# Optimization experiments

Hardware: AMD Instinct MI355X
Metric: run time of the kernel (lower is better)

## Reference

```python
import jax, jax.numpy as jnp
import numpy as np

B, L, C = 256, 196, 2048   # batch, conv_att_size, conv_feat_size
E, H, A = 512, 512, 512    # input_encoding_size, lstm_size, att_hidden_size
INITRANGE = 0.1


def _uniform(key, shape):
    return jax.random.uniform(key, shape, jnp.float32, -INITRANGE, INITRANGE)


def setup_inputs() -> dict:
    key = jax.random.key(0)
    ks = jax.random.split(key, 16)
    return {
        "xt": jax.random.normal(ks[0], (B, E), jnp.float32),
        "att_seq": jax.random.normal(ks[1], (B, L, C), jnp.float32),
        "h0": jax.random.normal(ks[2], (1, B, H), jnp.float32),
        "c0": jax.random.normal(ks[3], (1, B, H), jnp.float32),
        # LSTM input projections
        "Wi": _uniform(ks[4], (4 * H, E)), "bi": _uniform(ks[5], (4 * H,)),
        "Wh": _uniform(ks[6], (4 * H, H)), "bh": _uniform(ks[7], (4 * H,)),
        "Wz": _uniform(ks[8], (4 * H, C)), "bz": _uniform(ks[9], (4 * H,)),
        # attention MLP
        "Wa": _uniform(ks[10], (A, C)), "ba": _uniform(ks[11], (A,)),
        "Wha": _uniform(ks[12], (A, H)), "bha": _uniform(ks[13], (A,)),
        "Wo": _uniform(ks[14], (1, A)), "bo": _uniform(ks[15], (1,)),
    }


def reference(xt, att_seq, h0, c0, Wi, bi, Wh, bh, Wz, bz, Wa, ba, Wha, bha, Wo, bo):
    pre_h = h0[-1]  # [B, H]
    pre_c = c0[-1]  # [B, H]

    # attention scoring MLP
    att_linear = jnp.einsum('blc,ac->bla', att_seq, Wa) + ba      # [B, L, A]
    h_linear = pre_h @ Wha.T + bha                                 # [B, A]
    att_h = jnp.tanh(att_linear + h_linear[:, None, :])            # [B, L, A]
    scores = jnp.einsum('bla,a->bl', att_h, Wo[0]) + bo[0]         # [B, L]
    conv_weight = jax.nn.softmax(scores, axis=1)                   # [B, L]

    # weighted sum over attention locations -> context z
    z = jnp.einsum('blc,bl->bc', att_seq, conv_weight)             # [B, C]

    # fused LSTM gates
    all_input_sums = (xt @ Wi.T + bi) + (pre_h @ Wh.T + bh) + (z @ Wz.T + bz)  # [B, 4H]
    gates = jax.nn.sigmoid(all_input_sums[:, :3 * H])
    in_gate = gates[:, :H]
    forget_gate = gates[:, H:2 * H]
    out_gate = gates[:, 2 * H:3 * H]
    in_transform = jnp.tanh(all_input_sums[:, 3 * H:])

    next_c = forget_gate * pre_c + in_gate * in_transform
    next_h = out_gate * jnp.tanh(next_c)
    # dropout is identity in eval mode (deterministic baseline)
    return next_h, next_c
```

## Files before the change

kernel.cpp:

```cpp
#include <hip/hip_runtime.h>
#include <stdint.h>

#define B_ 256
#define L_ 196
#define C_ 2048
#define E_ 512
#define H_ 512
#define A_ 512
#define M_ (B_*L_)

typedef __bf16 bf16x8 __attribute__((ext_vector_type(8)));
typedef float  f32x4  __attribute__((ext_vector_type(4)));

__device__ __forceinline__ unsigned short f2bf(float f) {
    union { float f; unsigned int u; } v; v.f = f;
    unsigned int r = 0x7FFFu + ((v.u >> 16) & 1u);
    return (unsigned short)((v.u + r) >> 16);
}

__device__ __forceinline__ unsigned int pk2(float a, float b) {
    return (unsigned int)f2bf(a) | ((unsigned int)f2bf(b) << 16);
}

__device__ __forceinline__ float tanh_fast(float x) {
    float e = __expf(2.f * x);
    return 1.f - 2.f / (e + 1.f);
}

__device__ __forceinline__ void gload_lds16(const void* g, void* s) {
    __builtin_amdgcn_global_load_lds(
        (const __attribute__((address_space(1))) void*)g,
        (__attribute__((address_space(3))) void*)s, 16, 0, 0);
}


__global__ void k_cvt(const float* __restrict__ src, unsigned short* __restrict__ dst, int n4) {
    int i = blockIdx.x * blockDim.x + threadIdx.x;
    if (i < n4) {
        float4 v = ((const float4*)src)[i];
        ushort4 o; o.x = f2bf(v.x); o.y = f2bf(v.y); o.z = f2bf(v.z); o.w = f2bf(v.w);
        ((ushort4*)dst)[i] = o;
    }
}

__global__ void k_build_wcat(const float* __restrict__ Wi, const float* __restrict__ Wh,
                             const float* __restrict__ Wz, const float* __restrict__ bi,
                             const float* __restrict__ bh, const float* __restrict__ bz,
                             unsigned short* __restrict__ wcat, float* __restrict__ bcat) {
    int j = blockIdx.x;
    int t = threadIdx.x;
    for (int g = t; g < 768; g += 256) {
        int k = g * 4;
        const float* src;
        if (k < 512)       src = Wi + j*512 + k;
        else if (k < 1024) src = Wh + j*512 + (k - 512);
        else               src = Wz + j*2048 + (k - 1024);
        float4 v = *(const float4*)src;
        ushort4 o; o.x = f2bf(v.x); o.y = f2bf(v.y); o.z = f2bf(v.z); o.w = f2bf(v.w);
        *(ushort4*)(wcat + (size_t)j*3072 + k) = o;
    }
    if (t == 0) bcat[j] = bi[j] + bh[j] + bz[j];
}

__global__ void k_build_xcat(const float* __restrict__ xt, const float* __restrict__ preh,
                             unsigned short* __restrict__ xcat) {
    int b = blockIdx.x, t = threadIdx.x;
    const float* src = (t < 128) ? (xt + b*512 + t*4) : (preh + b*512 + (t-128)*4);
    int off = (t < 128) ? (t*4) : (512 + (t-128)*4);
    float4 v = *(const float4*)src;
    ushort4 o; o.x = f2bf(v.x); o.y = f2bf(v.y); o.z = f2bf(v.z); o.w = f2bf(v.w);
    *(ushort4*)(xcat + (size_t)b*3072 + off) = o;
}

__global__ void k_hlin(const float* __restrict__ preh, const float* __restrict__ Wha,
                       const float* __restrict__ bha, const float* __restrict__ ba,
                       float* __restrict__ hlin) {
    __shared__ float ph[512];
    int b = blockIdx.x, t = threadIdx.x;
    ph[t] = preh[b*512 + t];
    __syncthreads();
    float acc = bha[t] + ba[t];
    const float4* wrow = (const float4*)(Wha + (size_t)t*512);
    #pragma unroll 8
    for (int k4 = 0; k4 < 128; ++k4) {
        float4 v = wrow[k4];
        float4 p = *(const float4*)&ph[k4*4];
        acc += v.x*p.x + v.y*p.y + v.z*p.z + v.w*p.w;
    }
    hlin[b*512 + t] = acc;
}


#define VWAIT8 asm volatile("s_waitcnt vmcnt(8)" ::: "memory")
#define VWAIT4 asm volatile("s_waitcnt vmcnt(4)" ::: "memory")
#define VWAIT0 asm volatile("s_waitcnt vmcnt(0)" ::: "memory")
#define LWAIT0 asm volatile("s_waitcnt lgkmcnt(0)" ::: "memory")

#define ISSUE_B(K0, LBN) do { \
    _Pragma("unroll") \
    for (int i_ = 0; i_ < 8; ++i_) \
        gload_lds16(wa + (size_t)(brow0 + i_*64)*C_ + (K0) + bpsC*8, \
                    (LBN) + (size_t)(tid + i_*512)*8); \
} while(0)

#define LOAD_A(K0) do { const float* ga_ = gaBase + (K0); \
    av0 = *(const float4*)(ga_);      av1 = *(const float4*)(ga_ + 4); \
    av2 = *(const float4*)(ga_ + 8);  av3 = *(const float4*)(ga_ + 12); \
} while(0)

#define PACK_A(LAN) do { \
    uint4 w0_ = make_uint4(pk2(av0.x,av0.y), pk2(av0.z,av0.w), pk2(av1.x,av1.y), pk2(av1.z,av1.w)); \
    uint4 w1_ = make_uint4(pk2(av2.x,av2.y), pk2(av2.z,av2.w), pk2(av3.x,av3.y), pk2(av3.z,av3.w)); \
    *(uint4*)&(LAN)[ar*64 + ((app     ^ ars) * 8)] = w0_; \
    *(uint4*)&(LAN)[ar*64 + (((app+1) ^ ars) * 8)] = w1_; \
} while(0)

#define COMPUTE(KK, LA, LB) do { \
    const int c_ = (KK)*4 + lq; \
    bf16x8 af_[4]; \
    _Pragma("unroll") \
    for (int m_ = 0; m_ < 4; ++m_) { \
        int rrow_ = wr*64 + m_*16 + l16; \
        af_[m_] = *(const bf16x8*)&(LA)[rrow_*64 + ((c_ ^ (rrow_ & 7)) * 8)]; } \
    __builtin_amdgcn_s_setprio(1); \
    _Pragma("unroll") \
    for (int n_ = 0; n_ < 8; ++n_) { \
        int brow_ = wc*128 + n_*16 + l16; \
        bf16x8 bf_ = *(const bf16x8*)&(LB)[brow_*64 + ((c_ ^ (brow_ & 7)) * 8)]; \
        _Pragma("unroll") \
        for (int m_ = 0; m_ < 4; ++m_) \
            acc[m_][n_] = __builtin_amdgcn_mfma_f32_16x16x32_bf16(af_[m_], bf_, acc[m_][n_], 0, 0, 0); } \
    __builtin_amdgcn_s_setprio(0); \
} while(0)

__global__ __launch_bounds__(512, 1) void k_scores(
    const float* __restrict__ att,
    const unsigned short* __restrict__ wa,
    const float* __restrict__ hlin,
    const float* __restrict__ wo,
    const float* __restrict__ bo,
    float* __restrict__ scores)
{
    __shared__ unsigned short smem[81920];
    const int tid = threadIdx.x;
    const int w = tid >> 6, l = tid & 63;
    const int l16 = l & 15, lq = l >> 4;
    const int wr = w >> 2, wc = w & 3;
    const int row0 = blockIdx.x * 128;

    const int ar = tid >> 2;
    const int app = (tid & 3) * 2;
    const int ars = ar & 7;
    const float* gaBase = att + (size_t)(row0 + ar)*C_ + app*8;

    const int brow0 = tid >> 3;
    const int bpsC = (tid & 7) ^ ((tid >> 3) & 7);

    f32x4 acc[4][8];
    #pragma unroll
    for (int m = 0; m < 4; ++m)
        #pragma unroll
        for (int n = 0; n < 8; ++n) acc[m][n] = (f32x4){0.f, 0.f, 0.f, 0.f};

    float4 av0, av1, av2, av3;
    unsigned short* lA0 = smem;
    unsigned short* lB0 = smem + 8192;
    unsigned short* lA1 = smem + 40960;
    unsigned short* lB1 = smem + 40960 + 8192;

    LOAD_A(0);
    ISSUE_B(0, lB0);
    VWAIT8;
    PACK_A(lA0);
    LOAD_A(64);
    VWAIT4;
    LWAIT0;
    __builtin_amdgcn_s_barrier();

    for (int kt = 0; kt < 30; ++kt) {
        unsigned short* lA  = (kt & 1) ? lA1 : lA0;
        unsigned short* lB  = (kt & 1) ? lB1 : lB0;
        unsigned short* lAn = (kt & 1) ? lA0 : lA1;
        unsigned short* lBn = (kt & 1) ? lB0 : lB1;
        ISSUE_B((kt + 1) * 64, lBn);
        COMPUTE(0, lA, lB);
        VWAIT8;
        PACK_A(lAn);
        COMPUTE(1, lA, lB);
        LOAD_A((kt + 2) * 64);
        VWAIT4;
        LWAIT0;
        __builtin_amdgcn_s_barrier();
    }

    {
        ISSUE_B(31 * 64, lB1);
        COMPUTE(0, lA0, lB0);
        VWAIT8;
        PACK_A(lA1);
        COMPUTE(1, lA0, lB0);
        VWAIT0;
        LWAIT0;
        __builtin_amdgcn_s_barrier();
    }

    COMPUTE(0, lA1, lB1);
    COMPUTE(1, lA1, lB1);

    __syncthreads();
    float* red = (float*)smem;

    const int colbase = wc*128 + l16;
    float won[8], hlA[8], hlB[8];
    const int bA = row0 / L_;
    const int bB = (row0 + 127) / L_;
    const int rsplit = (bA + 1) * L_;
    #pragma unroll
    for (int n = 0; n < 8; ++n) {
        won[n] = wo[colbase + n*16];
        hlA[n] = hlin[bA*A_ + colbase + n*16];
        hlB[n] = hlin[bB*A_ + colbase + n*16];
    }

    #pragma unroll
    for (int m = 0; m < 4; ++m) {
        #pragma unroll
        for (int r = 0; r < 4; ++r) {
            int lrow = wr*64 + m*16 + lq*4 + r;
            int grow = row0 + lrow;
            bool useB = grow >= rsplit;
            float s = 0.f;
            #pragma unroll
            for (int n = 0; n < 8; ++n) {
                float v = acc[m][n][r] + (useB ? hlB[n] : hlA[n]);
                s += tanh_fast(v) * won[n];
            }
            s += __shfl_xor(s, 1);
            s += __shfl_xor(s, 2);
            s += __shfl_xor(s, 4);
            s += __shfl_xor(s, 8);
            if (l16 == 0) red[wc*128 + lrow] = s;
        }
    }
    __syncthreads();
    if (tid < 128) {
        scores[row0 + tid] = red[tid] + red[128 + tid] + red[256 + tid] + red[384 + tid] + bo[0];
    }
}

__global__ void k_softmax(const float* __restrict__ scores, float* __restrict__ cw) {
    __shared__ float sm[4], ss[4];
    int b = blockIdx.x, t = threadIdx.x, w = t >> 6, l = t & 63;
    float v = (t < L_) ? scores[b*L_ + t] : -1e30f;
    float m = v;
    #pragma unroll
    for (int o = 1; o < 64; o <<= 1) m = fmaxf(m, __shfl_xor(m, o));
    if (l == 0) sm[w] = m;
    __syncthreads();
    m = fmaxf(fmaxf(sm[0], sm[1]), fmaxf(sm[2], sm[3]));
    float e = (t < L_) ? expf(v - m) : 0.f;
    float s = e;
    #pragma unroll
    for (int o = 1; o < 64; o <<= 1) s += __shfl_xor(s, o);
    if (l == 0) ss[w] = s;
    __syncthreads();
    s = ss[0] + ss[1] + ss[2] + ss[3];
    if (t < L_) cw[b*L_ + t] = e / s;
}

__global__ void k_z(const float* __restrict__ att, const float* __restrict__ cw,
                    unsigned short* __restrict__ xcat) {
    __shared__ float w_s[L_];
    int b = blockIdx.y, half = blockIdx.x, t = threadIdx.x;
    if (t < L_) w_s[t] = cw[b*L_ + t];
    __syncthreads();
    int c = half*1024 + t*4;
    const float* base = att + (size_t)b*L_*C_ + c;
    float ax = 0.f, ay = 0.f, az = 0.f, aw = 0.f;
    #pragma unroll 4
    for (int li = 0; li < L_; ++li) {
        float4 v = *(const float4*)(base + (size_t)li*C_);
        float wt = w_s[li];
        ax += wt*v.x; ay += wt*v.y; az += wt*v.z; aw += wt*v.w;
    }
    ushort4 o; o.x = f2bf(ax); o.y = f2bf(ay); o.z = f2bf(az); o.w = f2bf(aw);
    *(ushort4*)(xcat + (size_t)b*3072 + 1024 + c) = o;
}

#define K2_LDK 40
__global__ __launch_bounds__(256) void k_gemm2(
    const unsigned short* __restrict__ xcat,
    const unsigned short* __restrict__ wcat,
    const float* __restrict__ bcat,
    float* __restrict__ S)
{
    __shared__ unsigned short lA[64 * K2_LDK];
    __shared__ unsigned short lB[128 * K2_LDK];
    const int tid = threadIdx.x;
    const int w = tid >> 6, l = tid & 63;
    const int l16 = l & 15, lq = l >> 4;
    const int row0 = blockIdx.y * 64;
    const int col0 = blockIdx.x * 128;

    f32x4 acc[4][2];
    #pragma unroll
    for (int m = 0; m < 4; ++m)
        #pragma unroll
        for (int n = 0; n < 2; ++n) acc[m][n] = (f32x4){0.f, 0.f, 0.f, 0.f};

    for (int kt = 0; kt < 3072/32; ++kt) {
        const int k0 = kt * 32;
        __syncthreads();
        {
            int r = tid >> 2, c8 = tid & 3;
            *(uint4*)&lA[r*K2_LDK + c8*8] =
                *(const uint4*)(xcat + (size_t)(row0 + r)*3072 + k0 + c8*8);
        }
        #pragma unroll
        for (int i = 0; i < 2; ++i) {
            int g = tid + i*256;
            int r = g >> 2, c8 = g & 3;
            *(uint4*)&lB[r*K2_LDK + c8*8] =
                *(const uint4*)(wcat + (size_t)(col0 + r)*3072 + k0 + c8*8);
        }
        __syncthreads();

        bf16x8 af[4];
        #pragma unroll
        for (int m = 0; m < 4; ++m)
            af[m] = *(const bf16x8*)&lA[(m*16 + l16)*K2_LDK + lq*8];
        #pragma unroll
        for (int n = 0; n < 2; ++n) {
            bf16x8 bfr = *(const bf16x8*)&lB[(w*32 + n*16 + l16)*K2_LDK + lq*8];
            #pragma unroll
            for (int m = 0; m < 4; ++m)
                acc[m][n] = __builtin_amdgcn_mfma_f32_16x16x32_bf16(af[m], bfr, acc[m][n], 0, 0, 0);
        }
    }

    #pragma unroll
    for (int m = 0; m < 4; ++m)
        #pragma unroll
        for (int n = 0; n < 2; ++n)
            #pragma unroll
            for (int r = 0; r < 4; ++r) {
                int grow = row0 + m*16 + lq*4 + r;
                int col = col0 + w*32 + n*16 + l16;
                S[(size_t)grow*2048 + col] = acc[m][n][r] + bcat[col];
            }
}

__global__ void k_lstm(const float* __restrict__ S, const float* __restrict__ prec,
                       float* __restrict__ out) {
    int b = blockIdx.x, h = threadIdx.x;
    float ig = 1.f / (1.f + expf(-S[(size_t)b*2048 + h]));
    float fg = 1.f / (1.f + expf(-S[(size_t)b*2048 + 512 + h]));
    float og = 1.f / (1.f + expf(-S[(size_t)b*2048 + 1024 + h]));
    float gt = tanhf(S[(size_t)b*2048 + 1536 + h]);
    float c = fg * prec[b*512 + h] + ig * gt;
    out[b*512 + h] = og * tanhf(c);
    out[131072 + b*512 + h] = c;
}

extern "C" void kernel_launch(void* const* d_in, const int* in_sizes, int n_in,
                              void* d_out, int out_size, void* d_ws, size_t ws_size,
                              hipStream_t stream) {
    const float* xt  = (const float*)d_in[0];
    const float* att = (const float*)d_in[1];
    const float* h0  = (const float*)d_in[2];
    const float* c0  = (const float*)d_in[3];
    const float* Wi  = (const float*)d_in[4];
    const float* bi  = (const float*)d_in[5];
    const float* Wh  = (const float*)d_in[6];
    const float* bh  = (const float*)d_in[7];
    const float* Wz  = (const float*)d_in[8];
    const float* bz  = (const float*)d_in[9];
    const float* Wa  = (const float*)d_in[10];
    const float* ba  = (const float*)d_in[11];
    const float* Wha = (const float*)d_in[12];
    const float* bha = (const float*)d_in[13];
    const float* Wo  = (const float*)d_in[14];
    const float* bo  = (const float*)d_in[15];
    float* out = (float*)d_out;

    char* ws = (char*)d_ws;
    unsigned short* wa_bf   = (unsigned short*)(ws);
    unsigned short* wcat_bf = (unsigned short*)(ws + 2097152);
    unsigned short* xcat_bf = (unsigned short*)(ws + 14680064);
    float* hlin   = (float*)(ws + 16252928);
    float* scores = (float*)(ws + 16777216);
    float* cw     = (float*)(ws + 16977920);
    float* bcat   = (float*)(ws + 17178624);
    float* S      = (float*)(ws + 17186816);

    k_cvt<<<1024, 256, 0, stream>>>(Wa, wa_bf, 262144);
    k_build_wcat<<<2048, 256, 0, stream>>>(Wi, Wh, Wz, bi, bh, bz, wcat_bf, bcat);
    k_build_xcat<<<256, 256, 0, stream>>>(xt, h0, xcat_bf);
    k_hlin<<<256, 512, 0, stream>>>(h0, Wha, bha, ba, hlin);
    k_scores<<<M_/128, 512, 0, stream>>>(att, wa_bf, hlin, Wo, bo, scores);
    k_softmax<<<256, 256, 0, stream>>>(scores, cw);
    k_z<<<dim3(2, 256), 256, 0, stream>>>(att, cw, xcat_bf);
    k_gemm2<<<dim3(16, 4), 256, 0, stream>>>(xcat_bf, wcat_bf, bcat, S);
    k_lstm<<<256, 512, 0, stream>>>(S, c0, out);
}
```

Baseline: 343.3 us.

## Split scores GEMM into 128x256 tiles with two column blocks and partial sums

The attention-score GEMM moves from 128x512 tiles with 512 threads and one block per CU to 128x256 tiles with 256 threads, a 32-wide K step, and two blocks per CU. The grid is remapped so that column blocks sharing a row block stay close together. Each column block writes a partial score, and the softmax kernel adds the two partials plus the bias. The aim is higher occupancy and better latency hiding from smaller LDS use. The cost is that the att activations are read and converted to bf16 twice, and each K step is shorter, so there are more barriers.

```diff
diff --git a/kernel.cpp b/kernel.cpp
--- a/kernel.cpp
+++ b/kernel.cpp
@@ -91,70 +91,78 @@
 }
 
 
-#define VWAIT8 asm volatile("s_waitcnt vmcnt(8)" ::: "memory")
 #define VWAIT4 asm volatile("s_waitcnt vmcnt(4)" ::: "memory")
 #define VWAIT0 asm volatile("s_waitcnt vmcnt(0)" ::: "memory")
 #define LWAIT0 asm volatile("s_waitcnt lgkmcnt(0)" ::: "memory")
 
 #define ISSUE_B(K0, LBN) do { \
     _Pragma("unroll") \
-    for (int i_ = 0; i_ < 8; ++i_) \
-        gload_lds16(wa + (size_t)(brow0 + i_*64)*C_ + (K0) + bpsC*8, \
-                    (LBN) + (size_t)(tid + i_*512)*8); \
+    for (int i_ = 0; i_ < 4; ++i_) \
+        gload_lds16(gbBase + (size_t)i_*64*C_ + (K0), \
+                    (LBN) + (size_t)(tid + i_*256)*8); \
 } while(0)
 
-#define LOAD_A(K0) do { const float* ga_ = gaBase + (K0); \
-    av0 = *(const float4*)(ga_);      av1 = *(const float4*)(ga_ + 4); \
-    av2 = *(const float4*)(ga_ + 8);  av3 = *(const float4*)(ga_ + 12); \
+#define LOAD_A(K0) do { \
+    av0 = *(const float4*)(gaBase0 + (K0));      av1 = *(const float4*)(gaBase0 + (K0) + 4); \
+    av2 = *(const float4*)(gaBase1 + (K0));      av3 = *(const float4*)(gaBase1 + (K0) + 4); \
 } while(0)
 
 #define PACK_A(LAN) do { \
     uint4 w0_ = make_uint4(pk2(av0.x,av0.y), pk2(av0.z,av0.w), pk2(av1.x,av1.y), pk2(av1.z,av1.w)); \
     uint4 w1_ = make_uint4(pk2(av2.x,av2.y), pk2(av2.z,av2.w), pk2(av3.x,av3.y), pk2(av3.z,av3.w)); \
-    *(uint4*)&(LAN)[ar*64 + ((app     ^ ars) * 8)] = w0_; \
-    *(uint4*)&(LAN)[ar*64 + (((app+1) ^ ars) * 8)] = w1_; \
+    *(uint4*)&(LAN)[ar0*32 + aqs] = w0_; \
+    *(uint4*)&(LAN)[ar0*32 + 2048 + aqs] = w1_; \
 } while(0)
 
-#define COMPUTE(KK, LA, LB) do { \
-    const int c_ = (KK)*4 + lq; \
+#define COMPUTE(LA, LB) do { \
     bf16x8 af_[4]; \
     _Pragma("unroll") \
-    for (int m_ = 0; m_ < 4; ++m_) { \
-        int rrow_ = wr*64 + m_*16 + l16; \
-        af_[m_] = *(const bf16x8*)&(LA)[rrow_*64 + ((c_ ^ (rrow_ & 7)) * 8)]; } \
+    for (int m_ = 0; m_ < 4; ++m_) \
+        af_[m_] = *(const bf16x8*)&(LA)[(wr*64 + m_*16 + l16)*32 + co]; \
     __builtin_amdgcn_s_setprio(1); \
     _Pragma("unroll") \
     for (int n_ = 0; n_ < 8; ++n_) { \
-        int brow_ = wc*128 + n_*16 + l16; \
-        bf16x8 bf_ = *(const bf16x8*)&(LB)[brow_*64 + ((c_ ^ (brow_ & 7)) * 8)]; \
+        bf16x8 bf_ = *(const bf16x8*)&(LB)[(wc*128 + n_*16 + l16)*32 + co]; \
         _Pragma("unroll") \
         for (int m_ = 0; m_ < 4; ++m_) \
             acc[m_][n_] = __builtin_amdgcn_mfma_f32_16x16x32_bf16(af_[m_], bf_, acc[m_][n_], 0, 0, 0); } \
     __builtin_amdgcn_s_setprio(0); \
 } while(0)
 
-__global__ __launch_bounds__(512, 1) void k_scores(
+__global__ __launch_bounds__(256, 2) void k_scores(
     const float* __restrict__ att,
     const unsigned short* __restrict__ wa,
     const float* __restrict__ hlin,
     const float* __restrict__ wo,
-    const float* __restrict__ bo,
-    float* __restrict__ scores)
+    float* __restrict__ part)
 {
-    __shared__ unsigned short smem[81920];
+    __shared__ unsigned short smem[24576];
     const int tid = threadIdx.x;
     const int w = tid >> 6, l = tid & 63;
     const int l16 = l & 15, lq = l >> 4;
-    const int wr = w >> 2, wc = w & 3;
-    const int row0 = blockIdx.x * 128;
-
-    const int ar = tid >> 2;
-    const int app = (tid & 3) * 2;
-    const int ars = ar & 7;
-    const float* gaBase = att + (size_t)(row0 + ar)*C_ + app*8;
-
-    const int brow0 = tid >> 3;
-    const int bpsC = (tid & 7) ^ ((tid >> 3) & 7);
+    const int wr = w >> 1, wc = w & 1;
+
+    const int orig = blockIdx.x;
+    const int wgid = (orig & 7) * 98 + (orig >> 3);
+    const int rowblk = wgid >> 1, colblk = wgid & 1;
+    const int row0 = rowblk * 128;
+    const int colB0 = colblk * 256;
+
+    const int ar0 = tid >> 2;
+    const int aq = tid & 3;
+    const int asw = (ar0 & 3) ^ ((ar0 >> 2) & 3);
+    const int aqs = ((aq ^ asw) << 3);
+    const float* gaBase0 = att + (size_t)(row0 + ar0)*C_ + aq*8;
+    const float* gaBase1 = gaBase0 + (size_t)64*C_;
+    const unsigned short* gbBase = wa + (size_t)(colB0 + ar0)*C_ + (aq ^ asw)*8;
+
+    const int lsw = (l16 & 3) ^ ((l16 >> 2) & 3);
+    const int co = ((lq ^ lsw) << 3);
+
+    unsigned short* lA0 = smem;
+    unsigned short* lB0 = smem + 4096;
+    unsigned short* lA1 = smem + 12288;
+    unsigned short* lB1 = smem + 12288 + 4096;
 
     f32x4 acc[4][8];
     #pragma unroll
@@ -163,54 +171,45 @@
         for (int n = 0; n < 8; ++n) acc[m][n] = (f32x4){0.f, 0.f, 0.f, 0.f};
 
     float4 av0, av1, av2, av3;
-    unsigned short* lA0 = smem;
-    unsigned short* lB0 = smem + 8192;
-    unsigned short* lA1 = smem + 40960;
-    unsigned short* lB1 = smem + 40960 + 8192;
 
     LOAD_A(0);
     ISSUE_B(0, lB0);
-    VWAIT8;
+    VWAIT4;
     PACK_A(lA0);
-    LOAD_A(64);
+    LOAD_A(32);
     VWAIT4;
     LWAIT0;
     __builtin_amdgcn_s_barrier();
 
-    for (int kt = 0; kt < 30; ++kt) {
+    for (int kt = 0; kt < 62; ++kt) {
         unsigned short* lA  = (kt & 1) ? lA1 : lA0;
         unsigned short* lB  = (kt & 1) ? lB1 : lB0;
         unsigned short* lAn = (kt & 1) ? lA0 : lA1;
         unsigned short* lBn = (kt & 1) ? lB0 : lB1;
-        ISSUE_B((kt + 1) * 64, lBn);
-        COMPUTE(0, lA, lB);
-        VWAIT8;
+        ISSUE_B((kt + 1) * 32, lBn);
+        VWAIT4;
         PACK_A(lAn);
-        COMPUTE(1, lA, lB);
-        LOAD_A((kt + 2) * 64);
+        COMPUTE(lA, lB);
+        LOAD_A((kt + 2) * 32);
         VWAIT4;
         LWAIT0;
         __builtin_amdgcn_s_barrier();
     }
 
-    {
-        ISSUE_B(31 * 64, lB1);
-        COMPUTE(0, lA0, lB0);
-        VWAIT8;
-        PACK_A(lA1);
-        COMPUTE(1, lA0, lB0);
-        VWAIT0;
-        LWAIT0;
-        __builtin_amdgcn_s_barrier();
-    }
-
-    COMPUTE(0, lA1, lB1);
-    COMPUTE(1, lA1, lB1);
+    ISSUE_B(63 * 32, lB1);
+    VWAIT4;
+    PACK_A(lA1);
+    COMPUTE(lA0, lB0);
+    VWAIT0;
+    LWAIT0;
+    __builtin_amdgcn_s_barrier();
+
+    COMPUTE(lA1, lB1);
 
     __syncthreads();
     float* red = (float*)smem;
 
-    const int colbase = wc*128 + l16;
+    const int colbase = colB0 + wc*128 + l16;
     float won[8], hlA[8], hlB[8];
     const int bA = row0 / L_;
     const int bB = (row0 + 127) / L_;
@@ -243,15 +242,19 @@
         }
     }
     __syncthreads();
-    if (tid < 128) {
-        scores[row0 + tid] = red[tid] + red[128 + tid] + red[256 + tid] + red[384 + tid] + bo[0];
-    }
-}
-
-__global__ void k_softmax(const float* __restrict__ scores, float* __restrict__ cw) {
+    if (tid < 128)
+        part[(size_t)colblk*M_ + row0 + tid] = red[tid] + red[128 + tid];
+}
+
+__global__ void k_softmax(const float* __restrict__ part, const float* __restrict__ bo,
+                          float* __restrict__ cw) {
     __shared__ float sm[4], ss[4];
     int b = blockIdx.x, t = threadIdx.x, w = t >> 6, l = t & 63;
-    float v = (t < L_) ? scores[b*L_ + t] : -1e30f;
+    float v = -1e30f;
+    if (t < L_) {
+        int idx = b*L_ + t;
+        v = part[idx] + part[M_ + idx] + bo[0];
+    }
     float m = v;
     #pragma unroll
     for (int o = 1; o < 64; o <<= 1) m = fmaxf(m, __shfl_xor(m, o));
@@ -388,17 +391,17 @@
     unsigned short* wcat_bf = (unsigned short*)(ws + 2097152);
     unsigned short* xcat_bf = (unsigned short*)(ws + 14680064);
     float* hlin   = (float*)(ws + 16252928);
-    float* scores = (float*)(ws + 16777216);
-    float* cw     = (float*)(ws + 16977920);
-    float* bcat   = (float*)(ws + 17178624);
-    float* S      = (float*)(ws + 17186816);
+    float* part   = (float*)(ws + 16777216);
+    float* cw     = (float*)(ws + 17825792);
+    float* bcat   = (float*)(ws + 18087936);
+    float* S      = (float*)(ws + 18096128);
 
     k_cvt<<<1024, 256, 0, stream>>>(Wa, wa_bf, 262144);
     k_build_wcat<<<2048, 256, 0, stream>>>(Wi, Wh, Wz, bi, bh, bz, wcat_bf, bcat);
     k_build_xcat<<<256, 256, 0, stream>>>(xt, h0, xcat_bf);
     k_hlin<<<256, 512, 0, stream>>>(h0, Wha, bha, ba, hlin);
-    k_scores<<<M_/128, 512, 0, stream>>>(att, wa_bf, hlin, Wo, bo, scores);
-    k_softmax<<<256, 256, 0, stream>>>(scores, cw);
+    k_scores<<<784, 256, 0, stream>>>(att, wa_bf, hlin, Wo, part);
+    k_softmax<<<256, 256, 0, stream>>>(part, bo, cw);
     k_z<<<dim3(2, 256), 256, 0, stream>>>(att, cw, xcat_bf);
     k_gemm2<<<dim3(16, 4), 256, 0, stream>>>(xcat_bf, wcat_bf, bcat, S);
     k_lstm<<<256, 512, 0, stream>>>(S, c0, out);
```

Result: slower. 426.5 us (+24.3%).

## Emit bf16 copy of att_seq from scores GEMM and read it in context reduction

Applied to the files above, without the earlier changes.

The scores kernel, which already converts att_seq tiles to bf16 for the MFMA, now also stores those bf16 tiles to a workspace buffer. The context-vector kernel then reads the bf16 copy instead of the fp32 tensor, halving its read traffic. The trade-off is an extra large global write inside the GEMM main loop and reduced precision of the weighted sum inputs.

```diff
diff --git a/kernel.cpp b/kernel.cpp
--- a/kernel.cpp
+++ b/kernel.cpp
@@ -20,6 +20,10 @@
 
 __device__ __forceinline__ unsigned int pk2(float a, float b) {
     return (unsigned int)f2bf(a) | ((unsigned int)f2bf(b) << 16);
+}
+
+__device__ __forceinline__ float bf2f(unsigned int lo16) {
+    union { unsigned int u; float f; } v; v.u = lo16 << 16; return v.f;
 }
 
 __device__ __forceinline__ float tanh_fast(float x) {
@@ -108,11 +112,13 @@
     av2 = *(const float4*)(ga_ + 8);  av3 = *(const float4*)(ga_ + 12); \
 } while(0)
 
-#define PACK_A(LAN) do { \
+#define PACK_STORE_A(LAN, KN) do { \
     uint4 w0_ = make_uint4(pk2(av0.x,av0.y), pk2(av0.z,av0.w), pk2(av1.x,av1.y), pk2(av1.z,av1.w)); \
     uint4 w1_ = make_uint4(pk2(av2.x,av2.y), pk2(av2.z,av2.w), pk2(av3.x,av3.y), pk2(av3.z,av3.w)); \
     *(uint4*)&(LAN)[ar*64 + ((app     ^ ars) * 8)] = w0_; \
     *(uint4*)&(LAN)[ar*64 + (((app+1) ^ ars) * 8)] = w1_; \
+    *(uint4*)&abf[(KN)]     = w0_; \
+    *(uint4*)&abf[(KN) + 8] = w1_; \
 } while(0)
 
 #define COMPUTE(KK, LA, LB) do { \
@@ -139,7 +145,8 @@
     const float* __restrict__ hlin,
     const float* __restrict__ wo,
     const float* __restrict__ bo,
-    float* __restrict__ scores)
+    float* __restrict__ scores,
+    unsigned short* __restrict__ attbf)
 {
     __shared__ unsigned short smem[81920];
     const int tid = threadIdx.x;
@@ -152,6 +159,7 @@
     const int app = (tid & 3) * 2;
     const int ars = ar & 7;
     const float* gaBase = att + (size_t)(row0 + ar)*C_ + app*8;
+    unsigned short* abf = attbf + (size_t)(row0 + ar)*C_ + app*8;
 
     const int brow0 = tid >> 3;
     const int bpsC = (tid & 7) ^ ((tid >> 3) & 7);
@@ -171,7 +179,7 @@
     LOAD_A(0);
     ISSUE_B(0, lB0);
     VWAIT8;
-    PACK_A(lA0);
+    PACK_STORE_A(lA0, 0);
     LOAD_A(64);
     VWAIT4;
     LWAIT0;
@@ -185,7 +193,7 @@
         ISSUE_B((kt + 1) * 64, lBn);
         COMPUTE(0, lA, lB);
         VWAIT8;
-        PACK_A(lAn);
+        PACK_STORE_A(lAn, (kt + 1) * 64);
         COMPUTE(1, lA, lB);
         LOAD_A((kt + 2) * 64);
         VWAIT4;
@@ -197,7 +205,7 @@
         ISSUE_B(31 * 64, lB1);
         COMPUTE(0, lA0, lB0);
         VWAIT8;
-        PACK_A(lA1);
+        PACK_STORE_A(lA1, 31 * 64);
         COMPUTE(1, lA0, lB0);
         VWAIT0;
         LWAIT0;
@@ -268,22 +276,25 @@
     if (t < L_) cw[b*L_ + t] = e / s;
 }
 
-__global__ void k_z(const float* __restrict__ att, const float* __restrict__ cw,
+__global__ void k_z(const unsigned short* __restrict__ attbf, const float* __restrict__ cw,
                     unsigned short* __restrict__ xcat) {
     __shared__ float w_s[L_];
     int b = blockIdx.y, half = blockIdx.x, t = threadIdx.x;
     if (t < L_) w_s[t] = cw[b*L_ + t];
     __syncthreads();
     int c = half*1024 + t*4;
-    const float* base = att + (size_t)b*L_*C_ + c;
-    float ax = 0.f, ay = 0.f, az = 0.f, aw = 0.f;
+    const unsigned short* base = attbf + (size_t)b*L_*C_ + c;
+    float a0 = 0.f, a1 = 0.f, a2 = 0.f, a3 = 0.f;
     #pragma unroll 4
     for (int li = 0; li < L_; ++li) {
-        float4 v = *(const float4*)(base + (size_t)li*C_);
+        uint2 v = *(const uint2*)(base + (size_t)li*C_);
         float wt = w_s[li];
-        ax += wt*v.x; ay += wt*v.y; az += wt*v.z; aw += wt*v.w;
-    }
-    ushort4 o; o.x = f2bf(ax); o.y = f2bf(ay); o.z = f2bf(az); o.w = f2bf(aw);
+        a0 += wt * bf2f(v.x & 0xffffu);
+        a1 += wt * bf2f(v.x >> 16);
+        a2 += wt * bf2f(v.y & 0xffffu);
+        a3 += wt * bf2f(v.y >> 16);
+    }
+    ushort4 o; o.x = f2bf(a0); o.y = f2bf(a1); o.z = f2bf(a2); o.w = f2bf(a3);
     *(ushort4*)(xcat + (size_t)b*3072 + 1024 + c) = o;
 }
 
@@ -392,14 +403,15 @@
     float* cw     = (float*)(ws + 16977920);
     float* bcat   = (float*)(ws + 17178624);
     float* S      = (float*)(ws + 17186816);
+    unsigned short* attbf = (unsigned short*)(ws + 33554432);
 
     k_cvt<<<1024, 256, 0, stream>>>(Wa, wa_bf, 262144);
     k_build_wcat<<<2048, 256, 0, stream>>>(Wi, Wh, Wz, bi, bh, bz, wcat_bf, bcat);
     k_build_xcat<<<256, 256, 0, stream>>>(xt, h0, xcat_bf);
     k_hlin<<<256, 512, 0, stream>>>(h0, Wha, bha, ba, hlin);
-    k_scores<<<M_/128, 512, 0, stream>>>(att, wa_bf, hlin, Wo, bo, scores);
+    k_scores<<<M_/128, 512, 0, stream>>>(att, wa_bf, hlin, Wo, bo, scores, attbf);
     k_softmax<<<256, 256, 0, stream>>>(scores, cw);
-    k_z<<<dim3(2, 256), 256, 0, stream>>>(att, cw, xcat_bf);
+    k_z<<<dim3(2, 256), 256, 0, stream>>>(attbf, cw, xcat_bf);
     k_gemm2<<<dim3(16, 4), 256, 0, stream>>>(xcat_bf, wcat_bf, bcat, S);
     k_lstm<<<256, 512, 0, stream>>>(S, c0, out);
 }
```

Result: slower. 377.4 us (+9.9%).

## Fuse prep kernels, deepen A prefetch in scores GEMM, split-K LSTM GEMM

Applied to the files above, without the earlier changes.

Merges the weight/input conversion and h-linear kernels into one launch to cut launch overhead. The attention-score GEMM now keeps two A tiles in flight in registers with an unrolled double-buffer loop to hide global load latency. The LSTM gate GEMM is split along K into two halves, uses direct global-to-LDS loads with an XOR-swizzled layout, and adds partials plus bias in the LSTM kernel. Extra register pressure and extra partial-sum traffic are the tradeoffs.

```diff
diff --git a/kernel.cpp b/kernel.cpp
--- a/kernel.cpp
+++ b/kernel.cpp
@@ -33,68 +33,72 @@
         (__attribute__((address_space(3))) void*)s, 16, 0, 0);
 }
 
-
-__global__ void k_cvt(const float* __restrict__ src, unsigned short* __restrict__ dst, int n4) {
-    int i = blockIdx.x * blockDim.x + threadIdx.x;
-    if (i < n4) {
-        float4 v = ((const float4*)src)[i];
+__global__ __launch_bounds__(256) void k_prep(
+    const float* __restrict__ Wa,
+    const float* __restrict__ Wi, const float* __restrict__ Wh,
+    const float* __restrict__ Wz, const float* __restrict__ bi,
+    const float* __restrict__ bh, const float* __restrict__ bz,
+    const float* __restrict__ xt, const float* __restrict__ preh,
+    const float* __restrict__ Wha, const float* __restrict__ bha,
+    const float* __restrict__ ba,
+    unsigned short* __restrict__ wa_bf, unsigned short* __restrict__ wcat,
+    float* __restrict__ bcat, unsigned short* __restrict__ xcat,
+    float* __restrict__ hlin)
+{
+    const int bid = blockIdx.x, t = threadIdx.x;
+    if (bid < 1024) {
+        int i = bid * 256 + t;
+        float4 v = ((const float4*)Wa)[i];
         ushort4 o; o.x = f2bf(v.x); o.y = f2bf(v.y); o.z = f2bf(v.z); o.w = f2bf(v.w);
-        ((ushort4*)dst)[i] = o;
-    }
-}
-
-__global__ void k_build_wcat(const float* __restrict__ Wi, const float* __restrict__ Wh,
-                             const float* __restrict__ Wz, const float* __restrict__ bi,
-                             const float* __restrict__ bh, const float* __restrict__ bz,
-                             unsigned short* __restrict__ wcat, float* __restrict__ bcat) {
-    int j = blockIdx.x;
-    int t = threadIdx.x;
-    for (int g = t; g < 768; g += 256) {
-        int k = g * 4;
-        const float* src;
-        if (k < 512)       src = Wi + j*512 + k;
-        else if (k < 1024) src = Wh + j*512 + (k - 512);
-        else               src = Wz + j*2048 + (k - 1024);
+        ((ushort4*)wa_bf)[i] = o;
+    } else if (bid < 3072) {
+        int j = bid - 1024;
+        for (int g = t; g < 768; g += 256) {
+            int k = g * 4;
+            const float* src;
+            if (k < 512)       src = Wi + j*512 + k;
+            else if (k < 1024) src = Wh + j*512 + (k - 512);
+            else               src = Wz + j*2048 + (k - 1024);
+            float4 v = *(const float4*)src;
+            ushort4 o; o.x = f2bf(v.x); o.y = f2bf(v.y); o.z = f2bf(v.z); o.w = f2bf(v.w);
+            *(ushort4*)(wcat + (size_t)j*3072 + k) = o;
+        }
+        if (t == 0) bcat[j] = bi[j] + bh[j] + bz[j];
+    } else if (bid < 3328) {
+        int b = bid - 3072;
+        const float* src = (t < 128) ? (xt + b*512 + t*4) : (preh + b*512 + (t-128)*4);
+        int off = (t < 128) ? (t*4) : (512 + (t-128)*4);
         float4 v = *(const float4*)src;
         ushort4 o; o.x = f2bf(v.x); o.y = f2bf(v.y); o.z = f2bf(v.z); o.w = f2bf(v.w);
-        *(ushort4*)(wcat + (size_t)j*3072 + k) = o;
-    }
-    if (t == 0) bcat[j] = bi[j] + bh[j] + bz[j];
-}
-
-__global__ void k_build_xcat(const float* __restrict__ xt, const float* __restrict__ preh,
-                             unsigned short* __restrict__ xcat) {
-    int b = blockIdx.x, t = threadIdx.x;
-    const float* src = (t < 128) ? (xt + b*512 + t*4) : (preh + b*512 + (t-128)*4);
-    int off = (t < 128) ? (t*4) : (512 + (t-128)*4);
-    float4 v = *(const float4*)src;
-    ushort4 o; o.x = f2bf(v.x); o.y = f2bf(v.y); o.z = f2bf(v.z); o.w = f2bf(v.w);
-    *(ushort4*)(xcat + (size_t)b*3072 + off) = o;
-}
-
-__global__ void k_hlin(const float* __restrict__ preh, const float* __restrict__ Wha,
-                       const float* __restrict__ bha, const float* __restrict__ ba,
-                       float* __restrict__ hlin) {
-    __shared__ float ph[512];
-    int b = blockIdx.x, t = threadIdx.x;
-    ph[t] = preh[b*512 + t];
-    __syncthreads();
-    float acc = bha[t] + ba[t];
-    const float4* wrow = (const float4*)(Wha + (size_t)t*512);
-    #pragma unroll 8
-    for (int k4 = 0; k4 < 128; ++k4) {
-        float4 v = wrow[k4];
-        float4 p = *(const float4*)&ph[k4*4];
-        acc += v.x*p.x + v.y*p.y + v.z*p.z + v.w*p.w;
-    }
-    hlin[b*512 + t] = acc;
-}
-
-
-#define VWAIT8 asm volatile("s_waitcnt vmcnt(8)" ::: "memory")
-#define VWAIT4 asm volatile("s_waitcnt vmcnt(4)" ::: "memory")
-#define VWAIT0 asm volatile("s_waitcnt vmcnt(0)" ::: "memory")
-#define LWAIT0 asm volatile("s_waitcnt lgkmcnt(0)" ::: "memory")
+        *(ushort4*)(xcat + (size_t)b*3072 + off) = o;
+    } else {
+        __shared__ float ph[512];
+        int b = bid - 3328;
+        ph[t] = preh[b*512 + t];
+        ph[t + 256] = preh[b*512 + t + 256];
+        __syncthreads();
+        #pragma unroll
+        for (int o = 0; o < 2; ++o) {
+            int a = t + o*256;
+            float acc = bha[a] + ba[a];
+            const float4* wrow = (const float4*)(Wha + (size_t)a*512);
+            #pragma unroll 8
+            for (int k4 = 0; k4 < 128; ++k4) {
+                float4 v = wrow[k4];
+                float4 p = *(const float4*)&ph[k4*4];
+                acc += v.x*p.x + v.y*p.y + v.z*p.z + v.w*p.w;
+            }
+            hlin[b*512 + a] = acc;
+        }
+    }
+}
+
+
+#define VWAIT12 asm volatile("s_waitcnt vmcnt(12)" ::: "memory")
+#define VWAIT8  asm volatile("s_waitcnt vmcnt(8)"  ::: "memory")
+#define VWAIT4  asm volatile("s_waitcnt vmcnt(4)"  ::: "memory")
+#define VWAIT0  asm volatile("s_waitcnt vmcnt(0)"  ::: "memory")
+#define LWAIT0  asm volatile("s_waitcnt lgkmcnt(0)" ::: "memory")
 
 #define ISSUE_B(K0, LBN) do { \
     _Pragma("unroll") \
@@ -103,14 +107,26 @@
                     (LBN) + (size_t)(tid + i_*512)*8); \
 } while(0)
 
-#define LOAD_A(K0) do { const float* ga_ = gaBase + (K0); \
-    av0 = *(const float4*)(ga_);      av1 = *(const float4*)(ga_ + 4); \
-    av2 = *(const float4*)(ga_ + 8);  av3 = *(const float4*)(ga_ + 12); \
-} while(0)
-
-#define PACK_A(LAN) do { \
-    uint4 w0_ = make_uint4(pk2(av0.x,av0.y), pk2(av0.z,av0.w), pk2(av1.x,av1.y), pk2(av1.z,av1.w)); \
-    uint4 w1_ = make_uint4(pk2(av2.x,av2.y), pk2(av2.z,av2.w), pk2(av3.x,av3.y), pk2(av3.z,av3.w)); \
+#define LOAD_A_A(K0) do { const float* ga_ = gaBase + (K0); \
+    a0 = *(const float4*)(ga_);      a1 = *(const float4*)(ga_ + 4); \
+    a2 = *(const float4*)(ga_ + 8);  a3 = *(const float4*)(ga_ + 12); \
+} while(0)
+
+#define LOAD_A_B(K0) do { const float* ga_ = gaBase + (K0); \
+    b0 = *(const float4*)(ga_);      b1 = *(const float4*)(ga_ + 4); \
+    b2 = *(const float4*)(ga_ + 8);  b3 = *(const float4*)(ga_ + 12); \
+} while(0)
+
+#define PACK_A_A(LAN) do { \
+    uint4 w0_ = make_uint4(pk2(a0.x,a0.y), pk2(a0.z,a0.w), pk2(a1.x,a1.y), pk2(a1.z,a1.w)); \
+    uint4 w1_ = make_uint4(pk2(a2.x,a2.y), pk2(a2.z,a2.w), pk2(a3.x,a3.y), pk2(a3.z,a3.w)); \
+    *(uint4*)&(LAN)[ar*64 + ((app     ^ ars) * 8)] = w0_; \
+    *(uint4*)&(LAN)[ar*64 + (((app+1) ^ ars) * 8)] = w1_; \
+} while(0)
+
+#define PACK_A_B(LAN) do { \
+    uint4 w0_ = make_uint4(pk2(b0.x,b0.y), pk2(b0.z,b0.w), pk2(b1.x,b1.y), pk2(b1.z,b1.w)); \
+    uint4 w1_ = make_uint4(pk2(b2.x,b2.y), pk2(b2.z,b2.w), pk2(b3.x,b3.y), pk2(b3.z,b3.w)); \
     *(uint4*)&(LAN)[ar*64 + ((app     ^ ars) * 8)] = w0_; \
     *(uint4*)&(LAN)[ar*64 + (((app+1) ^ ars) * 8)] = w1_; \
 } while(0)
@@ -162,32 +178,39 @@
         #pragma unroll
         for (int n = 0; n < 8; ++n) acc[m][n] = (f32x4){0.f, 0.f, 0.f, 0.f};
 
-    float4 av0, av1, av2, av3;
+    float4 a0, a1, a2, a3;
+    float4 b0, b1, b2, b3;
     unsigned short* lA0 = smem;
     unsigned short* lB0 = smem + 8192;
     unsigned short* lA1 = smem + 40960;
     unsigned short* lB1 = smem + 40960 + 8192;
 
-    LOAD_A(0);
+    LOAD_A_A(0);
     ISSUE_B(0, lB0);
-    VWAIT8;
-    PACK_A(lA0);
-    LOAD_A(64);
+    LOAD_A_B(64);
+    VWAIT12;
+    PACK_A_A(lA0);
     VWAIT4;
     LWAIT0;
     __builtin_amdgcn_s_barrier();
 
-    for (int kt = 0; kt < 30; ++kt) {
-        unsigned short* lA  = (kt & 1) ? lA1 : lA0;
-        unsigned short* lB  = (kt & 1) ? lB1 : lB0;
-        unsigned short* lAn = (kt & 1) ? lA0 : lA1;
-        unsigned short* lBn = (kt & 1) ? lB0 : lB1;
-        ISSUE_B((kt + 1) * 64, lBn);
-        COMPUTE(0, lA, lB);
-        VWAIT8;
-        PACK_A(lAn);
-        COMPUTE(1, lA, lB);
-        LOAD_A((kt + 2) * 64);
+    for (int kt2 = 0; kt2 < 15; ++kt2) {
+        const int kt = kt2 * 2;
+        ISSUE_B((kt + 1) * 64, lB1);
+        LOAD_A_A((kt + 2) * 64);
+        COMPUTE(0, lA0, lB0);
+        VWAIT12;
+        PACK_A_B(lA1);
+        COMPUTE(1, lA0, lB0);
+        VWAIT4;
+        LWAIT0;
+        __builtin_amdgcn_s_barrier();
+        ISSUE_B((kt + 2) * 64, lB0);
+        LOAD_A_B((kt + 3) * 64);
+        COMPUTE(0, lA1, lB1);
+        VWAIT12;
+        PACK_A_A(lA0);
+        COMPUTE(1, lA1, lB1);
         VWAIT4;
         LWAIT0;
         __builtin_amdgcn_s_barrier();
@@ -197,7 +220,7 @@
         ISSUE_B(31 * 64, lB1);
         COMPUTE(0, lA0, lB0);
         VWAIT8;
-        PACK_A(lA1);
+        PACK_A_B(lA1);
         COMPUTE(1, lA0, lB0);
         VWAIT0;
         LWAIT0;
@@ -287,76 +310,92 @@
     *(ushort4*)(xcat + (size_t)b*3072 + 1024 + c) = o;
 }
 
-#define K2_LDK 40
 __global__ __launch_bounds__(256) void k_gemm2(
     const unsigned short* __restrict__ xcat,
     const unsigned short* __restrict__ wcat,
-    const float* __restrict__ bcat,
-    float* __restrict__ S)
+    float* __restrict__ Sp)
 {
-    __shared__ unsigned short lA[64 * K2_LDK];
-    __shared__ unsigned short lB[128 * K2_LDK];
+    __shared__ unsigned short smem[12288];
+    unsigned short* lA = smem;
+    unsigned short* lB = smem + 4096;
     const int tid = threadIdx.x;
     const int w = tid >> 6, l = tid & 63;
     const int l16 = l & 15, lq = l >> 4;
+    const int wr = w >> 1, wc = w & 1;
     const int row0 = blockIdx.y * 64;
     const int col0 = blockIdx.x * 128;
-
-    f32x4 acc[4][2];
-    #pragma unroll
-    for (int m = 0; m < 4; ++m)
-        #pragma unroll
-        for (int n = 0; n < 2; ++n) acc[m][n] = (f32x4){0.f, 0.f, 0.f, 0.f};
-
-    for (int kt = 0; kt < 3072/32; ++kt) {
-        const int k0 = kt * 32;
+    const int half = blockIdx.z;
+    const int kbase = half * 1536;
+
+    f32x4 acc[2][4];
+    #pragma unroll
+    for (int m = 0; m < 2; ++m)
+        #pragma unroll
+        for (int n = 0; n < 4; ++n) acc[m][n] = (f32x4){0.f, 0.f, 0.f, 0.f};
+
+    for (int kt = 0; kt < 24; ++kt) {
+        const int k0 = kbase + kt * 64;
         __syncthreads();
-        {
-            int r = tid >> 2, c8 = tid & 3;
-            *(uint4*)&lA[r*K2_LDK + c8*8] =
-                *(const uint4*)(xcat + (size_t)(row0 + r)*3072 + k0 + c8*8);
-        }
         #pragma unroll
         for (int i = 0; i < 2; ++i) {
             int g = tid + i*256;
-            int r = g >> 2, c8 = g & 3;
-            *(uint4*)&lB[r*K2_LDK + c8*8] =
-                *(const uint4*)(wcat + (size_t)(col0 + r)*3072 + k0 + c8*8);
+            int r = g >> 3, c = (g & 7) ^ (r & 7);
+            gload_lds16(xcat + (size_t)(row0 + r)*3072 + k0 + c*8, lA + (size_t)g*8);
+        }
+        #pragma unroll
+        for (int i = 0; i < 4; ++i) {
+            int g = tid + i*256;
+            int r = g >> 3, c = (g & 7) ^ (r & 7);
+            gload_lds16(wcat + (size_t)(col0 + r)*3072 + k0 + c*8, lB + (size_t)g*8);
         }
         __syncthreads();
 
-        bf16x8 af[4];
-        #pragma unroll
-        for (int m = 0; m < 4; ++m)
-            af[m] = *(const bf16x8*)&lA[(m*16 + l16)*K2_LDK + lq*8];
-        #pragma unroll
-        for (int n = 0; n < 2; ++n) {
-            bf16x8 bfr = *(const bf16x8*)&lB[(w*32 + n*16 + l16)*K2_LDK + lq*8];
+        #pragma unroll
+        for (int kk = 0; kk < 2; ++kk) {
+            const int c = kk*4 + lq;
+            bf16x8 af[2];
             #pragma unroll
-            for (int m = 0; m < 4; ++m)
-                acc[m][n] = __builtin_amdgcn_mfma_f32_16x16x32_bf16(af[m], bfr, acc[m][n], 0, 0, 0);
-        }
-    }
-
-    #pragma unroll
-    for (int m = 0; m < 4; ++m)
-        #pragma unroll
-        for (int n = 0; n < 2; ++n)
+            for (int m = 0; m < 2; ++m) {
+                int rrow = wr*32 + m*16 + l16;
+                af[m] = *(const bf16x8*)&lA[rrow*64 + ((c ^ (rrow & 7)) * 8)];
+            }
+            #pragma unroll
+            for (int n = 0; n < 4; ++n) {
+                int brow = wc*64 + n*16 + l16;
+                bf16x8 bfr = *(const bf16x8*)&lB[brow*64 + ((c ^ (brow & 7)) * 8)];
+                #pragma unroll
+                for (int m = 0; m < 2; ++m)
+                    acc[m][n] = __builtin_amdgcn_mfma_f32_16x16x32_bf16(af[m], bfr, acc[m][n], 0, 0, 0);
+            }
+        }
+    }
+
+    #pragma unroll
+    for (int m = 0; m < 2; ++m)
+        #pragma unroll
+        for (int n = 0; n < 4; ++n)
             #pragma unroll
             for (int r = 0; r < 4; ++r) {
-                int grow = row0 + m*16 + lq*4 + r;
-                int col = col0 + w*32 + n*16 + l16;
-                S[(size_t)grow*2048 + col] = acc[m][n][r] + bcat[col];
+                int grow = row0 + wr*32 + m*16 + lq*4 + r;
+                int col = col0 + wc*64 + n*16 + l16;
+                Sp[(size_t)half*524288 + (size_t)grow*2048 + col] = acc[m][n][r];
             }
 }
 
-__global__ void k_lstm(const float* __restrict__ S, const float* __restrict__ prec,
-                       float* __restrict__ out) {
+__global__ void k_lstm(const float* __restrict__ Sp, const float* __restrict__ bcat,
+                       const float* __restrict__ prec, float* __restrict__ out) {
     int b = blockIdx.x, h = threadIdx.x;
-    float ig = 1.f / (1.f + expf(-S[(size_t)b*2048 + h]));
-    float fg = 1.f / (1.f + expf(-S[(size_t)b*2048 + 512 + h]));
-    float og = 1.f / (1.f + expf(-S[(size_t)b*2048 + 1024 + h]));
-    float gt = tanhf(S[(size_t)b*2048 + 1536 + h]);
+    const float* S0 = Sp;
+    const float* S1 = Sp + 524288;
+    size_t base = (size_t)b*2048;
+    float si = S0[base + h]        + S1[base + h]        + bcat[h];
+    float sf = S0[base + 512 + h]  + S1[base + 512 + h]  + bcat[512 + h];
+    float so = S0[base + 1024 + h] + S1[base + 1024 + h] + bcat[1024 + h];
+    float sg = S0[base + 1536 + h] + S1[base + 1536 + h] + bcat[1536 + h];
+    float ig = 1.f / (1.f + expf(-si));
+    float fg = 1.f / (1.f + expf(-sf));
+    float og = 1.f / (1.f + expf(-so));
+    float gt = tanhf(sg);
     float c = fg * prec[b*512 + h] + ig * gt;
     out[b*512 + h] = og * tanhf(c);
     out[131072 + b*512 + h] = c;
@@ -391,15 +430,13 @@
     float* scores = (float*)(ws + 16777216);
     float* cw     = (float*)(ws + 16977920);
     float* bcat   = (float*)(ws + 17178624);
-    float* S      = (float*)(ws + 17186816);
-
-    k_cvt<<<1024, 256, 0, stream>>>(Wa, wa_bf, 262144);
-    k_build_wcat<<<2048, 256, 0, stream>>>(Wi, Wh, Wz, bi, bh, bz, wcat_bf, bcat);
-    k_build_xcat<<<256, 256, 0, stream>>>(xt, h0, xcat_bf);
-    k_hlin<<<256, 512, 0, stream>>>(h0, Wha, bha, ba, hlin);
+    float* Sp     = (float*)(ws + 17186816);
+
+    k_prep<<<3584, 256, 0, stream>>>(Wa, Wi, Wh, Wz, bi, bh, bz, xt, h0,
+                                     Wha, bha, ba, wa_bf, wcat_bf, bcat, xcat_bf, hlin);
     k_scores<<<M_/128, 512, 0, stream>>>(att, wa_bf, hlin, Wo, bo, scores);
     k_softmax<<<256, 256, 0, stream>>>(scores, cw);
     k_z<<<dim3(2, 256), 256, 0, stream>>>(att, cw, xcat_bf);
-    k_gemm2<<<dim3(16, 4), 256, 0, stream>>>(xcat_bf, wcat_bf, bcat, S);
-    k_lstm<<<256, 512, 0, stream>>>(S, c0, out);
-}
+    k_gemm2<<<dim3(16, 4, 2), 256, 0, stream>>>(xcat_bf, wcat_bf, Sp);
+    k_lstm<<<256, 512, 0, stream>>>(Sp, bcat, c0, out);
+}
```

After: 389.1 us. 13.3% more time.
